# Kernel optimization log

Hardware: AMD Instinct MI355X
Metric: run time of the kernel (lower is better)

Reference implementation:

```python
import jax, jax.numpy as jnp
import numpy as np

N, E, H, D_IN, L, G, T = 50000, 800000, 64, 64, 4, 128, 1

def _w(key, shape, fan_in):
    return jax.random.normal(key, shape, dtype=jnp.float32) / np.sqrt(fan_in)

def setup_inputs() -> dict:
    key = jax.random.key(0)
    ks = jax.random.split(key, 24)
    inp = {
        'x': jax.random.normal(ks[0], (N, D_IN), dtype=jnp.float32),
        'w': jax.random.normal(ks[1], (E, 1), dtype=jnp.float32),
        'src': jax.random.randint(ks[2], (E,), 0, N, dtype=jnp.int32),
        'dst': jax.random.randint(ks[3], (E,), 0, N, dtype=jnp.int32),
        'graph_id': jnp.sort(jax.random.randint(ks[4], (N,), 0, G, dtype=jnp.int32)),
        # input MLP (1 layer, last_activation None; SiLU applied in input_node_func)
        'W_in': _w(ks[5], (D_IN, H), D_IN), 'b_in': jnp.zeros((H,), jnp.float32),
        # per-layer message MLP: (2H+1 -> H -> H), SiLU mid and last
        'msg_W1': _w(ks[6], (L, 2 * H + 1, H), 2 * H + 1), 'msg_b1': jnp.zeros((L, H), jnp.float32),
        'msg_W2': _w(ks[7], (L, H, H), H), 'msg_b2': jnp.zeros((L, H), jnp.float32),
        # per-layer update MLP: (H -> H -> H), SiLU mid, last None
        'upd_W1': _w(ks[8], (L, H, H), H), 'upd_b1': jnp.zeros((L, H), jnp.float32),
        'upd_W2': _w(ks[9], (L, H, H), H), 'upd_b2': jnp.zeros((L, H), jnp.float32),
        # node-wise output MLP: (H -> H -> H), SiLU mid, last None
        'out_W1': _w(ks[10], (H, H), H), 'out_b1': jnp.zeros((H,), jnp.float32),
        'out_W2': _w(ks[11], (H, H), H), 'out_b2': jnp.zeros((H,), jnp.float32),
        # readout MLP: (3H -> H -> T), SiLU mid, last None
        'ro_W1': _w(ks[12], (3 * H, H), 3 * H), 'ro_b1': jnp.zeros((H,), jnp.float32),
        'ro_W2': _w(ks[13], (H, T), H), 'ro_b2': jnp.zeros((T,), jnp.float32),
    }
    return inp

def reference(x, w, src, dst, graph_id, W_in, b_in, msg_W1, msg_b1, msg_W2, msg_b2,
              upd_W1, upd_b1, upd_W2, upd_b2, out_W1, out_b1, out_W2, out_b2,
              ro_W1, ro_b1, ro_W2, ro_b2):
    silu = jax.nn.silu
    f = silu(x @ W_in + b_in)                                   # [N, H]
    sq = w * w                                                  # [E, 1]
    for l in range(L):
        mi = jnp.concatenate([f[src], f[dst], sq], axis=-1)     # [E, 2H+1]
        msg = silu(silu(mi @ msg_W1[l] + msg_b1[l]) @ msg_W2[l] + msg_b2[l])
        m = msg * jax.nn.sigmoid(msg)                           # gated message
        m_sum = jax.ops.segment_sum(m, dst, num_segments=N)     # scatter-sum to dst
        h_new = silu((m_sum + f) @ upd_W1[l] + upd_b1[l]) @ upd_W2[l] + upd_b2[l]
        f = h_new + f                                           # residual
    f = silu(f @ out_W1 + out_b1) @ out_W2 + out_b2             # node-wise output
    g_sum = jax.ops.segment_sum(f, graph_id, num_segments=G)
    cnt = jax.ops.segment_sum(jnp.ones((N, 1), f.dtype), graph_id, num_segments=G)
    g_mean = g_sum / jnp.maximum(cnt, 1.0)
    g_max = jax.ops.segment_max(f, graph_id, num_segments=G)
    readout = jnp.concatenate([g_sum, g_mean, g_max], axis=-1)  # [G, 3H]
    return silu(readout @ ro_W1 + ro_b1) @ ro_W2 + ro_b2        # [G, T]
```

## Files before the change

kernel.cpp:

```cpp
#include <hip/hip_runtime.h>

#define NN 50000
#define EE 800000
#define GG 128
#define LL 4
#define SCAN_B 196

typedef __bf16 bf16x8 __attribute__((ext_vector_type(8)));
typedef float  f32x4  __attribute__((ext_vector_type(4)));

__device__ __forceinline__ float silu_f(float x){
    float t = __builtin_amdgcn_exp2f(-1.44269504f * x);
    return x * __builtin_amdgcn_rcpf(1.0f + t);
}
__device__ __forceinline__ unsigned fenc(float v){
    unsigned u = __float_as_uint(v);
    return (u & 0x80000000u) ? ~u : (u | 0x80000000u);
}
__device__ __forceinline__ float fdec(unsigned u){
    return (u & 0x80000000u) ? __uint_as_float(u & 0x7fffffffu) : __uint_as_float(~u);
}

__global__ __launch_bounds__(256) void pack_k(
        const float* __restrict__ msgW1, const float* __restrict__ msgW2,
        const float* __restrict__ updW1, const float* __restrict__ updW2,
        const float* __restrict__ outW1, const float* __restrict__ outW2,
        const float* __restrict__ W_in, __bf16* __restrict__ pk){
    int m = blockIdx.x;
    const float* src;
    if(m<20){
        int l=m/5, r=m%5;
        if(r==0)      src = msgW1 + (size_t)l*129*64;
        else if(r==1) src = msgW1 + (size_t)l*129*64 + 64*64;
        else if(r==2) src = msgW2 + (size_t)l*64*64;
        else if(r==3) src = updW1 + (size_t)l*64*64;
        else          src = updW2 + (size_t)l*64*64;
    } else if(m==20) src=outW1; else if(m==21) src=outW2; else src=W_in;
    __bf16* dst = pk + (size_t)m*4096;
    int tid=threadIdx.x;
    #pragma unroll
    for(int i=0;i<16;++i){
        int idx = tid*16+i;
        int frag = idx>>9, lane=(idx>>3)&63, j=idx&7;
        int s=frag>>2, ng=frag&3, q=lane>>4, nn=lane&15;
        dst[idx] = (__bf16)src[(32*s+8*q+j)*64 + 16*ng + nn];
    }
}
__device__ __forceinline__ bf16x8 ldfrag(const __bf16* pk, int s, int ng, int lane){
    return *(const bf16x8*)&pk[(((s*4+ng)*64 + lane))*8];
}

__global__ __launch_bounds__(256) void input_mfma(const float* __restrict__ x,
        const __bf16* __restrict__ pkW, const float* __restrict__ bg,
        float* __restrict__ f, __bf16* __restrict__ f16, int N){
    int tid=threadIdx.x, wid=tid>>6, lane=tid&63;
    int q=lane>>4, nn=lane&15;
    bf16x8 Bf[2][4];
    #pragma unroll
    for(int s=0;s<2;++s)
        #pragma unroll
        for(int ng=0;ng<4;++ng) Bf[s][ng]=ldfrag(pkW,s,ng,lane);
    float bias[4];
    #pragma unroll
    for(int ng=0;ng<4;++ng) bias[ng]=bg[16*ng+nn];

    int ntiles=(N+15)/16;
    int gw=gridDim.x*4;
    for(int t=blockIdx.x*4+wid; t<ntiles; t+=gw){
        int m=t*16+nn; int mc=(m<N)?m:(N-1);
        float4 a0=*(const float4*)&x[(size_t)mc*64 + 8*q];
        float4 a1=*(const float4*)&x[(size_t)mc*64 + 8*q + 4];
        float4 a2=*(const float4*)&x[(size_t)mc*64 + 32 + 8*q];
        float4 a3=*(const float4*)&x[(size_t)mc*64 + 32 + 8*q + 4];
        bf16x8 af0, af1;
        af0[0]=(__bf16)a0.x; af0[1]=(__bf16)a0.y; af0[2]=(__bf16)a0.z; af0[3]=(__bf16)a0.w;
        af0[4]=(__bf16)a1.x; af0[5]=(__bf16)a1.y; af0[6]=(__bf16)a1.z; af0[7]=(__bf16)a1.w;
        af1[0]=(__bf16)a2.x; af1[1]=(__bf16)a2.y; af1[2]=(__bf16)a2.z; af1[3]=(__bf16)a2.w;
        af1[4]=(__bf16)a3.x; af1[5]=(__bf16)a3.y; af1[6]=(__bf16)a3.z; af1[7]=(__bf16)a3.w;
        #pragma unroll
        for(int ng=0;ng<4;++ng){
            f32x4 acc; acc[0]=bias[ng]; acc[1]=bias[ng]; acc[2]=bias[ng]; acc[3]=bias[ng];
            acc=__builtin_amdgcn_mfma_f32_16x16x32_bf16(af0,Bf[0][ng],acc,0,0,0);
            acc=__builtin_amdgcn_mfma_f32_16x16x32_bf16(af1,Bf[1][ng],acc,0,0,0);
            #pragma unroll
            for(int r=0;r<4;++r){
                int row=t*16+4*q+r;
                if(row<N){
                    float o=silu_f(acc[r]);
                    f[(size_t)row*64+16*ng+nn]=o;
                    f16[(size_t)row*64+16*ng+nn]=(__bf16)o;
                }
            }
        }
    }
}

__global__ void hist_k(const int* __restrict__ dst, int* __restrict__ deg, int E){
    int e=blockIdx.x*blockDim.x+threadIdx.x;
    if(e<E) atomicAdd(&deg[dst[e]],1);
}

__global__ __launch_bounds__(256) void scan1_k(const int* __restrict__ deg, int* __restrict__ curs,
        int* __restrict__ bsum, int N){
    __shared__ int sv[256];
    int tid=threadIdx.x;
    int idx=blockIdx.x*256+tid;
    int v=(idx<N)?deg[idx]:0;
    sv[tid]=v; __syncthreads();
    #pragma unroll
    for(int off=1; off<256; off<<=1){
        int a=(tid>=off)?sv[tid-off]:0;
        __syncthreads(); sv[tid]+=a; __syncthreads();
    }
    if(idx<N) curs[idx]=sv[tid]-v;
    if(tid==255) bsum[blockIdx.x]=sv[255];
}
__global__ __launch_bounds__(256) void scan2_k(int* __restrict__ bsum, int B){
    __shared__ int sv[256];
    int tid=threadIdx.x;
    int v=(tid<B)?bsum[tid]:0;
    sv[tid]=v; __syncthreads();
    #pragma unroll
    for(int off=1; off<256; off<<=1){
        int a=(tid>=off)?sv[tid-off]:0;
        __syncthreads(); sv[tid]+=a; __syncthreads();
    }
    if(tid<B) bsum[tid]=sv[tid]-v;
}
__global__ __launch_bounds__(256) void scan3_k(int* __restrict__ curs, const int* __restrict__ bsum, int N){
    int idx=blockIdx.x*256+threadIdx.x;
    if(idx<N) curs[idx]+=bsum[blockIdx.x];
}

__global__ void fill_k(const int* __restrict__ src, const int* __restrict__ dst,
                       const float* __restrict__ w, int* __restrict__ cursor,
                       int4* __restrict__ meta, int E){
    int e=blockIdx.x*blockDim.x+threadIdx.x;
    if(e<E){
        int d=dst[e];
        int r=atomicAdd(&cursor[d],1);
        float ww=w[e];
        int4 v; v.x=src[e]; v.y=d; v.z=__float_as_int(ww*ww); v.w=0;
        meta[r]=v;
    }
}

__global__ __launch_bounds__(256) void xy_mfma(const __bf16* __restrict__ f16,
        const __bf16* __restrict__ pkA, const __bf16* __restrict__ pkB,
        const float* __restrict__ b1, __bf16* __restrict__ XY, int N){
    int tid=threadIdx.x, wid=tid>>6, lane=tid&63;
    int q=lane>>4, nn=lane&15;
    bf16x8 Bf[2][8];
    #pragma unroll
    for(int s=0;s<2;++s){
        #pragma unroll
        for(int ng=0;ng<4;++ng){ Bf[s][ng]=ldfrag(pkA,s,ng,lane); Bf[s][4+ng]=ldfrag(pkB,s,ng,lane); }
    }
    float bias[8];
    #pragma unroll
    for(int ng=0;ng<8;++ng) bias[ng]=(ng<4)?0.f:b1[16*(ng-4)+nn];
    int ntiles=(N+15)/16;
    int gw=gridDim.x*4;
    for(int t=blockIdx.x*4+wid; t<ntiles; t+=gw){
        int row=t*16+nn; if(row>=N) row=N-1;
        bf16x8 a0=*(const bf16x8*)&f16[(size_t)row*64 + 8*q];
        bf16x8 a1=*(const bf16x8*)&f16[(size_t)row*64 + 32 + 8*q];
        #pragma unroll
        for(int ng=0;ng<8;++ng){
            f32x4 acc; acc[0]=bias[ng]; acc[1]=bias[ng]; acc[2]=bias[ng]; acc[3]=bias[ng];
            acc=__builtin_amdgcn_mfma_f32_16x16x32_bf16(a0,Bf[0][ng],acc,0,0,0);
            acc=__builtin_amdgcn_mfma_f32_16x16x32_bf16(a1,Bf[1][ng],acc,0,0,0);
            #pragma unroll
            for(int r=0;r<4;++r){
                int orow=t*16+4*q+r;
                if(orow<N) XY[(size_t)orow*128 + 16*ng + nn]=(__bf16)acc[r];
            }
        }
    }
}

__global__ __launch_bounds__(256) void edge_mfma3(
        const __bf16* __restrict__ XY, const int4* __restrict__ meta,
        const __bf16* __restrict__ pkW2,
        const float* __restrict__ W1, const float* __restrict__ b2,
        float* __restrict__ msum, int E){
    int tid=threadIdx.x, wid=tid>>6, lane=tid&63;
    int q=lane>>4, nn=lane&15;

    bf16x8 B2f[2][4];
    #pragma unroll
    for(int s=0;s<2;++s)
        #pragma unroll
        for(int ng=0;ng<4;++ng) B2f[s][ng]=ldfrag(pkW2,s,ng,lane);
    float w128lo[8], w128hi[8];
    #pragma unroll
    for(int j=0;j<8;++j){
        w128lo[j]=W1[128*64 + 8*q+j];
        w128hi[j]=W1[128*64 + 32+8*q+j];
    }
    float bias2[4];
    #pragma unroll
    for(int ng=0;ng<4;++ng) bias2[ng]=b2[16*ng+nn];

    __shared__ __bf16 sm16[4][32][66];

    int ntiles=E/32;
    int nw=gridDim.x*4;
    int chunk=(ntiles+nw-1)/nw;
    int wgl=blockIdx.x*4+wid;
    int t0=wgl*chunk, t1=t0+chunk; if(t1>ntiles) t1=ntiles;
    if(t0>=t1) return;

    int4 mv = meta[(size_t)t0*32 + (lane&31)];
    bf16x8 gx0lo,gx0hi,gy0lo,gy0hi,gx1lo,gx1hi,gy1lo,gy1hi;
    {
        int se0=__shfl(mv.x, nn,64),    de0=__shfl(mv.y, nn,64);
        int se1=__shfl(mv.x, 16+nn,64), de1=__shfl(mv.y, 16+nn,64);
        const __bf16* xp0=XY+(size_t)se0*128; const __bf16* yp0=XY+(size_t)de0*128+64;
        const __bf16* xp1=XY+(size_t)se1*128; const __bf16* yp1=XY+(size_t)de1*128+64;
        gx0lo=*(const bf16x8*)(xp0+8*q); gx0hi=*(const bf16x8*)(xp0+32+8*q);
        gy0lo=*(const bf16x8*)(yp0+8*q); gy0hi=*(const bf16x8*)(yp0+32+8*q);
        gx1lo=*(const bf16x8*)(xp1+8*q); gx1hi=*(const bf16x8*)(xp1+32+8*q);
        gy1lo=*(const bf16x8*)(yp1+8*q); gy1hi=*(const bf16x8*)(yp1+32+8*q);
    }
    int cur=__builtin_amdgcn_readlane(mv.y, 0);
    float vsum=0.f;

    for(int t=t0;t<t1;++t){
        bool hasn = (t+1<t1);
        int4 mvn = mv;
        if(hasn) mvn = meta[(size_t)(t+1)*32 + (lane&31)];

        int d_ = mv.y;
        float w2v = __int_as_float(mv.z);

        {
            float w2 = __shfl(w2v, nn, 64);
            bf16x8 a20, a21;
            #pragma unroll
            for(int j=0;j<8;++j){
                float hlo=(float)gx0lo[j] + (float)gy0lo[j] + w2*w128lo[j];
                float hhi=(float)gx0hi[j] + (float)gy0hi[j] + w2*w128hi[j];
                a20[j]=(__bf16)silu_f(hlo);
                a21[j]=(__bf16)silu_f(hhi);
            }
            f32x4 acc2[4];
            #pragma unroll
            for(int ng=0;ng<4;++ng){ f32x4 c; c[0]=bias2[ng]; c[1]=bias2[ng]; c[2]=bias2[ng]; c[3]=bias2[ng]; acc2[ng]=c; }
            #pragma unroll
            for(int ng=0;ng<4;++ng){
                acc2[ng]=__builtin_amdgcn_mfma_f32_16x16x32_bf16(a20,B2f[0][ng],acc2[ng],0,0,0);
                acc2[ng]=__builtin_amdgcn_mfma_f32_16x16x32_bf16(a21,B2f[1][ng],acc2[ng],0,0,0);
            }
            #pragma unroll
            for(int ng=0;ng<4;++ng)
                #pragma unroll
                for(int r=0;r<4;++r)
                    sm16[wid][4*q+r][16*ng+nn]=(__bf16)silu_f(silu_f(acc2[ng][r]));
        }
        {
            float w2 = __shfl(w2v, 16+nn, 64);
            bf16x8 a20, a21;
            #pragma unroll
            for(int j=0;j<8;++j){
                float hlo=(float)gx1lo[j] + (float)gy1lo[j] + w2*w128lo[j];
                float hhi=(float)gx1hi[j] + (float)gy1hi[j] + w2*w128hi[j];
                a20[j]=(__bf16)silu_f(hlo);
                a21[j]=(__bf16)silu_f(hhi);
            }
            f32x4 acc2[4];
            #pragma unroll
            for(int ng=0;ng<4;++ng){ f32x4 c; c[0]=bias2[ng]; c[1]=bias2[ng]; c[2]=bias2[ng]; c[3]=bias2[ng]; acc2[ng]=c; }
            #pragma unroll
            for(int ng=0;ng<4;++ng){
                acc2[ng]=__builtin_amdgcn_mfma_f32_16x16x32_bf16(a20,B2f[0][ng],acc2[ng],0,0,0);
                acc2[ng]=__builtin_amdgcn_mfma_f32_16x16x32_bf16(a21,B2f[1][ng],acc2[ng],0,0,0);
            }
            #pragma unroll
            for(int ng=0;ng<4;++ng)
                #pragma unroll
                for(int r=0;r<4;++r)
                    sm16[wid][16+4*q+r][16*ng+nn]=(__bf16)silu_f(silu_f(acc2[ng][r]));
        }
        asm volatile("" ::: "memory");

        if(hasn){
            int se0=__shfl(mvn.x, nn,64),    de0=__shfl(mvn.y, nn,64);
            int se1=__shfl(mvn.x, 16+nn,64), de1=__shfl(mvn.y, 16+nn,64);
            const __bf16* xp0=XY+(size_t)se0*128; const __bf16* yp0=XY+(size_t)de0*128+64;
            const __bf16* xp1=XY+(size_t)se1*128; const __bf16* yp1=XY+(size_t)de1*128+64;
            gx0lo=*(const bf16x8*)(xp0+8*q); gx0hi=*(const bf16x8*)(xp0+32+8*q);
            gy0lo=*(const bf16x8*)(yp0+8*q); gy0hi=*(const bf16x8*)(yp0+32+8*q);
            gx1lo=*(const bf16x8*)(xp1+8*q); gx1hi=*(const bf16x8*)(xp1+32+8*q);
            gy1lo=*(const bf16x8*)(yp1+8*q); gy1hi=*(const bf16x8*)(yp1+32+8*q);
        }

        #pragma unroll
        for(int r=0;r<32;++r){
            int dr=__builtin_amdgcn_readlane(d_, r);
            if(dr!=cur){
                atomicAdd(&msum[(size_t)cur*64+lane], vsum);
                vsum=0.f; cur=dr;
            }
            vsum+=(float)sm16[wid][r][lane];
        }
        asm volatile("" ::: "memory");
        mv = mvn;
    }
    atomicAdd(&msum[(size_t)cur*64+lane], vsum);
}

__global__ __launch_bounds__(256) void node_mfma(const float* __restrict__ A, const float* __restrict__ F,
        const __bf16* __restrict__ pkW1, const float* __restrict__ b1,
        const __bf16* __restrict__ pkW2, const float* __restrict__ b2,
        float* __restrict__ out, __bf16* __restrict__ out16, int N){
    int tid=threadIdx.x, wid=tid>>6, lane=tid&63;
    int q=lane>>4, nn=lane&15;

    bf16x8 B1f[2][4], B2f[2][4];
    #pragma unroll
    for(int s=0;s<2;++s)
        #pragma unroll
        for(int ng=0;ng<4;++ng){ B1f[s][ng]=ldfrag(pkW1,s,ng,lane); B2f[s][ng]=ldfrag(pkW2,s,ng,lane); }
    float bias1[4], bias2[4];
    #pragma unroll
    for(int ng=0;ng<4;++ng){ bias1[ng]=b1[16*ng+nn]; bias2[ng]=b2[16*ng+nn]; }

    __shared__ __align__(16) __bf16 sh1[4][16][72];
    __shared__ __align__(16) float sF[4][16][68];
    bool hasF = (F != nullptr);

    int ntiles=(N+15)/16;
    int gw=gridDim.x*4;
    for(int t=blockIdx.x*4+wid; t<ntiles; t+=gw){
        int m=t*16+nn;
        int mc=(m<N)?m:(N-1);
        float4 a0=*(const float4*)&A[(size_t)mc*64 + 8*q];
        float4 a1=*(const float4*)&A[(size_t)mc*64 + 8*q + 4];
        float4 a2=*(const float4*)&A[(size_t)mc*64 + 32 + 8*q];
        float4 a3=*(const float4*)&A[(size_t)mc*64 + 32 + 8*q + 4];
        if(hasF){
            float4 f0=*(const float4*)&F[(size_t)mc*64 + 8*q];
            float4 f1=*(const float4*)&F[(size_t)mc*64 + 8*q + 4];
            float4 f2_=*(const float4*)&F[(size_t)mc*64 + 32 + 8*q];
            float4 f3=*(const float4*)&F[(size_t)mc*64 + 32 + 8*q + 4];
            a0.x+=f0.x; a0.y+=f0.y; a0.z+=f0.z; a0.w+=f0.w;
            a1.x+=f1.x; a1.y+=f1.y; a1.z+=f1.z; a1.w+=f1.w;
            a2.x+=f2_.x; a2.y+=f2_.y; a2.z+=f2_.z; a2.w+=f2_.w;
            a3.x+=f3.x; a3.y+=f3.y; a3.z+=f3.z; a3.w+=f3.w;
            *(float4*)&sF[wid][nn][8*q]   = f0;
            *(float4*)&sF[wid][nn][8*q+4] = f1;
            *(float4*)&sF[wid][nn][32+8*q]   = f2_;
            *(float4*)&sF[wid][nn][32+8*q+4] = f3;
        }
        bf16x8 af0, af1;
        af0[0]=(__bf16)a0.x; af0[1]=(__bf16)a0.y; af0[2]=(__bf16)a0.z; af0[3]=(__bf16)a0.w;
        af0[4]=(__bf16)a1.x; af0[5]=(__bf16)a1.y; af0[6]=(__bf16)a1.z; af0[7]=(__bf16)a1.w;
        af1[0]=(__bf16)a2.x; af1[1]=(__bf16)a2.y; af1[2]=(__bf16)a2.z; af1[3]=(__bf16)a2.w;
        af1[4]=(__bf16)a3.x; af1[5]=(__bf16)a3.y; af1[6]=(__bf16)a3.z; af1[7]=(__bf16)a3.w;

        f32x4 acc[4];
        #pragma unroll
        for(int ng=0;ng<4;++ng){ f32x4 c; c[0]=bias1[ng]; c[1]=bias1[ng]; c[2]=bias1[ng]; c[3]=bias1[ng]; acc[ng]=c; }
        #pragma unroll
        for(int ng=0;ng<4;++ng){
            acc[ng]=__builtin_amdgcn_mfma_f32_16x16x32_bf16(af0,B1f[0][ng],acc[ng],0,0,0);
            acc[ng]=__builtin_amdgcn_mfma_f32_16x16x32_bf16(af1,B1f[1][ng],acc[ng],0,0,0);
        }
        #pragma unroll
        for(int ng=0;ng<4;++ng)
            #pragma unroll
            for(int r=0;r<4;++r)
                sh1[wid][4*q+r][16*ng+nn]=(__bf16)silu_f(acc[ng][r]);
        asm volatile("" ::: "memory");
        bf16x8 a20=*(const bf16x8*)&sh1[wid][nn][8*q];
        bf16x8 a21=*(const bf16x8*)&sh1[wid][nn][32+8*q];
        f32x4 acc2[4];
        #pragma unroll
        for(int ng=0;ng<4;++ng){ f32x4 c; c[0]=bias2[ng]; c[1]=bias2[ng]; c[2]=bias2[ng]; c[3]=bias2[ng]; acc2[ng]=c; }
        #pragma unroll
        for(int ng=0;ng<4;++ng){
            acc2[ng]=__builtin_amdgcn_mfma_f32_16x16x32_bf16(a20,B2f[0][ng],acc2[ng],0,0,0);
            acc2[ng]=__builtin_amdgcn_mfma_f32_16x16x32_bf16(a21,B2f[1][ng],acc2[ng],0,0,0);
        }
        #pragma unroll
        for(int ng=0;ng<4;++ng)
            #pragma unroll
            for(int r=0;r<4;++r){
                int row=t*16+4*q+r;
                if(row<N){
                    float o=acc2[ng][r];
                    if(hasF) o += sF[wid][4*q+r][16*ng+nn];
                    out[(size_t)row*64 + 16*ng + nn]=o;
                    if(out16) out16[(size_t)row*64 + 16*ng + nn]=(__bf16)o;
                }
            }
        asm volatile("" ::: "memory");
    }
}

__global__ __launch_bounds__(256) void seg_reduce_sorted(const float* __restrict__ f2, const int* __restrict__ gid,
        float* __restrict__ gsum, unsigned* __restrict__ gmaxu, float* __restrict__ cnt, int N){
    int wgl=blockIdx.x*4 + (threadIdx.x>>6);
    int lane=threadIdx.x&63;
    int W=gridDim.x*4;
    int chunk=(N+W-1)/W;
    int n0=wgl*chunk;
    int n1=n0+chunk; if(n1>N) n1=N;
    if(n0>=n1) return;
    int cur=gid[n0];
    float s=0.f, mx=-__builtin_inff(), c=0.f;
    for(int n=n0;n<n1;++n){
        int g=gid[n];
        float v=f2[(size_t)n*64+lane];
        if(g!=cur){
            atomicAdd(&gsum[(size_t)cur*64+lane], s);
            atomicMax(&gmaxu[(size_t)cur*64+lane], fenc(mx));
            if(lane==0) atomicAdd(&cnt[cur], c);
            s=0.f; mx=-__builtin_inff(); c=0.f; cur=g;
        }
        s+=v; mx=fmaxf(mx,v); c+=1.f;
    }
    atomicAdd(&gsum[(size_t)cur*64+lane], s);
    atomicMax(&gmaxu[(size_t)cur*64+lane], fenc(mx));
    if(lane==0) atomicAdd(&cnt[cur], c);
}

__global__ __launch_bounds__(256) void readout_k(const float* __restrict__ gsum, const unsigned* __restrict__ gmaxu,
        const float* __restrict__ cnt,
        const float* __restrict__ W1, const float* __restrict__ b1,
        const float* __restrict__ W2, const float* __restrict__ b2,
        float* __restrict__ out, int G){
    __shared__ __align__(16) float sr[4][192];
    int tid=threadIdx.x, wid=tid>>6, lane=tid&63;
    int g=blockIdx.x*4+wid;
    if(g<G){
        float s_=gsum[g*64+lane];
        float c=cnt[g];
        float mean=s_/fmaxf(c,1.0f);
        float mx=fdec(gmaxu[g*64+lane]);
        sr[wid][lane]=s_; sr[wid][64+lane]=mean; sr[wid][128+lane]=mx;
    }
    __syncthreads();
    if(g<G){
        float h=b1[lane];
        for(int k=0;k<192;k+=4){
            float4 r4=*(const float4*)&sr[wid][k];
            h += r4.x*W1[(k+0)*64+lane] + r4.y*W1[(k+1)*64+lane]
               + r4.z*W1[(k+2)*64+lane] + r4.w*W1[(k+3)*64+lane];
        }
        h=silu_f(h);
        float p=h*W2[lane];
        #pragma unroll
        for(int off=32;off>0;off>>=1) p += __shfl_down(p, off, 64);
        if(lane==0) out[g]=p+b2[0];
    }
}

extern "C" void kernel_launch(void* const* d_in, const int* in_sizes, int n_in,
                              void* d_out, int out_size, void* d_ws, size_t ws_size,
                              hipStream_t stream){
    const float* x     = (const float*)d_in[0];
    const float* w     = (const float*)d_in[1];
    const int*   src   = (const int*)d_in[2];
    const int*   dst   = (const int*)d_in[3];
    const int*   gid   = (const int*)d_in[4];
    const float* W_in  = (const float*)d_in[5];
    const float* b_in  = (const float*)d_in[6];
    const float* msgW1 = (const float*)d_in[7];
    const float* msgb1 = (const float*)d_in[8];
    const float* msgW2 = (const float*)d_in[9];
    const float* msgb2 = (const float*)d_in[10];
    const float* updW1 = (const float*)d_in[11];
    const float* updb1 = (const float*)d_in[12];
    const float* updW2 = (const float*)d_in[13];
    const float* updb2 = (const float*)d_in[14];
    const float* outW1 = (const float*)d_in[15];
    const float* outb1 = (const float*)d_in[16];
    const float* outW2 = (const float*)d_in[17];
    const float* outb2 = (const float*)d_in[18];
    const float* roW1  = (const float*)d_in[19];
    const float* rob1  = (const float*)d_in[20];
    const float* roW2  = (const float*)d_in[21];
    const float* rob2  = (const float*)d_in[22];

    float*  f     = (float*)d_ws;
    float*  msum  = f + (size_t)NN*64;
    float*  f2    = msum;
    __bf16* f16   = (__bf16*)(msum + (size_t)NN*64);
    __bf16* XY    = f16 + (size_t)NN*64;
    int4*   meta  = (int4*)(XY + (size_t)NN*128);
    __bf16* pk    = (__bf16*)(meta + EE);
    int*    deg   = (int*)(pk + 23*4096);
    int*    curs  = deg + 50048;
    int*    bsum  = curs + 50048;
    float*  gsum  = (float*)(bsum + 256);
    unsigned* gmaxu = (unsigned*)(gsum + GG*64);
    float*  cnt   = (float*)(gmaxu + GG*64);

    pack_k<<<dim3(23),dim3(256),0,stream>>>(msgW1, msgW2, updW1, updW2, outW1, outW2, W_in, pk);

    hipMemsetAsync(deg, 0, 50048*sizeof(int), stream);
    hist_k<<<dim3((EE+255)/256),dim3(256),0,stream>>>(dst, deg, EE);
    scan1_k<<<dim3(SCAN_B),dim3(256),0,stream>>>(deg, curs, bsum, NN);
    scan2_k<<<dim3(1),dim3(256),0,stream>>>(bsum, SCAN_B);
    scan3_k<<<dim3(SCAN_B),dim3(256),0,stream>>>(curs, bsum, NN);
    fill_k<<<dim3((EE+255)/256),dim3(256),0,stream>>>(src, dst, w, curs, meta, EE);

    input_mfma<<<dim3(782),dim3(256),0,stream>>>(x, pk + (size_t)22*4096, b_in, f, f16, NN);
    for(int l=0;l<LL;++l){
        xy_mfma<<<dim3(512),dim3(256),0,stream>>>(f16,
            pk + (size_t)(5*l+0)*4096, pk + (size_t)(5*l+1)*4096, msgb1 + l*64, XY, NN);
        hipMemsetAsync(msum, 0, (size_t)NN*64*sizeof(float), stream);
        edge_mfma3<<<dim3(1024),dim3(256),0,stream>>>(XY, meta,
            pk + (size_t)(5*l+2)*4096,
            msgW1 + (size_t)l*129*64, msgb2 + l*64, msum, EE);
        node_mfma<<<dim3(782),dim3(256),0,stream>>>(msum, f,
            pk + (size_t)(5*l+3)*4096, updb1 + l*64,
            pk + (size_t)(5*l+4)*4096, updb2 + l*64, f, f16, NN);
    }
    node_mfma<<<dim3(782),dim3(256),0,stream>>>(f, nullptr,
        pk + (size_t)20*4096, outb1, pk + (size_t)21*4096, outb2, f2, nullptr, NN);
    hipMemsetAsync(gsum, 0, (size_t)(GG*64*2 + GG)*sizeof(float), stream);
    seg_reduce_sorted<<<dim3(256),dim3(256),0,stream>>>(f2, gid, gsum, gmaxu, cnt, NN);
    readout_k<<<dim3(32),dim3(256),0,stream>>>(gsum, gmaxu, cnt, roW1, rob1, roW2, rob2, (float*)d_out, GG);
}
```

Measured before the change: 575.2 us.

## Fuse msum zeroing into xy kernel and restructure edge kernel pipeline

Removes the per-layer hipMemsetAsync of the message-sum buffer by zeroing it inside xy_mfma, whose grid is raised to one 16-row tile per wave. The edge kernel now computes both halves' first-layer activations before issuing the next tile's gathers, then runs the MFMAs. It writes results to shared memory as packed 4-wide bf16 stores in a permuted column layout, read back through a lane-to-column remap. The edge grid is doubled, giving shorter per-wave chunks, more parallelism and more boundary atomics.

```diff
diff --git a/kernel.cpp b/kernel.cpp
--- a/kernel.cpp
+++ b/kernel.cpp
@@ -7,6 +7,7 @@
 #define SCAN_B 196
 
 typedef __bf16 bf16x8 __attribute__((ext_vector_type(8)));
+typedef __bf16 bf16x4 __attribute__((ext_vector_type(4)));
 typedef float  f32x4  __attribute__((ext_vector_type(4)));
 
 __device__ __forceinline__ float silu_f(float x){
@@ -147,7 +148,8 @@
 
 __global__ __launch_bounds__(256) void xy_mfma(const __bf16* __restrict__ f16,
         const __bf16* __restrict__ pkA, const __bf16* __restrict__ pkB,
-        const float* __restrict__ b1, __bf16* __restrict__ XY, int N){
+        const float* __restrict__ b1, __bf16* __restrict__ XY,
+        float* __restrict__ msum, int N){
     int tid=threadIdx.x, wid=tid>>6, lane=tid&63;
     int q=lane>>4, nn=lane&15;
     bf16x8 Bf[2][8];
@@ -165,6 +167,17 @@
         int row=t*16+nn; if(row>=N) row=N-1;
         bf16x8 a0=*(const bf16x8*)&f16[(size_t)row*64 + 8*q];
         bf16x8 a1=*(const bf16x8*)&f16[(size_t)row*64 + 32 + 8*q];
+        {
+            float4 z; z.x=0.f; z.y=0.f; z.z=0.f; z.w=0.f;
+            float4* mz=(float4*)(msum + (size_t)t*1024);
+            int lim=(t*16+16<=N)?4:0;
+            if(lim){
+                #pragma unroll
+                for(int i=0;i<4;++i) mz[i*64+lane]=z;
+            } else {
+                for(int rr=t*16; rr<N; ++rr) msum[(size_t)rr*64+lane]=0.f;
+            }
+        }
         #pragma unroll
         for(int ng=0;ng<8;++ng){
             f32x4 acc; acc[0]=bias[ng]; acc[1]=bias[ng]; acc[2]=bias[ng]; acc[3]=bias[ng];
@@ -179,7 +192,7 @@
     }
 }
 
-__global__ __launch_bounds__(256) void edge_mfma3(
+__global__ __launch_bounds__(256) void edge_mfma4(
         const __bf16* __restrict__ XY, const int4* __restrict__ meta,
         const __bf16* __restrict__ pkW2,
         const float* __restrict__ W1, const float* __restrict__ b2,
@@ -202,7 +215,8 @@
     #pragma unroll
     for(int ng=0;ng<4;++ng) bias2[ng]=b2[16*ng+nn];
 
-    __shared__ __bf16 sm16[4][32][66];
+    __shared__ __align__(16) __bf16 sm16[4][32][68];
+    int cpos = 4*(lane&15) + (lane>>4);
 
     int ntiles=E/32;
     int nw=gridDim.x*4;
@@ -234,56 +248,18 @@
         int d_ = mv.y;
         float w2v = __int_as_float(mv.z);
 
+        bf16x8 A0lo,A0hi,A1lo,A1hi;
         {
-            float w2 = __shfl(w2v, nn, 64);
-            bf16x8 a20, a21;
+            float w2a = __shfl(w2v, nn, 64);
+            float w2b = __shfl(w2v, 16+nn, 64);
             #pragma unroll
             for(int j=0;j<8;++j){
-                float hlo=(float)gx0lo[j] + (float)gy0lo[j] + w2*w128lo[j];
-                float hhi=(float)gx0hi[j] + (float)gy0hi[j] + w2*w128hi[j];
-                a20[j]=(__bf16)silu_f(hlo);
-                a21[j]=(__bf16)silu_f(hhi);
-            }
-            f32x4 acc2[4];
-            #pragma unroll
-            for(int ng=0;ng<4;++ng){ f32x4 c; c[0]=bias2[ng]; c[1]=bias2[ng]; c[2]=bias2[ng]; c[3]=bias2[ng]; acc2[ng]=c; }
-            #pragma unroll
-            for(int ng=0;ng<4;++ng){
-                acc2[ng]=__builtin_amdgcn_mfma_f32_16x16x32_bf16(a20,B2f[0][ng],acc2[ng],0,0,0);
-                acc2[ng]=__builtin_amdgcn_mfma_f32_16x16x32_bf16(a21,B2f[1][ng],acc2[ng],0,0,0);
-            }
-            #pragma unroll
-            for(int ng=0;ng<4;++ng)
-                #pragma unroll
-                for(int r=0;r<4;++r)
-                    sm16[wid][4*q+r][16*ng+nn]=(__bf16)silu_f(silu_f(acc2[ng][r]));
-        }
-        {
-            float w2 = __shfl(w2v, 16+nn, 64);
-            bf16x8 a20, a21;
-            #pragma unroll
-            for(int j=0;j<8;++j){
-                float hlo=(float)gx1lo[j] + (float)gy1lo[j] + w2*w128lo[j];
-                float hhi=(float)gx1hi[j] + (float)gy1hi[j] + w2*w128hi[j];
-                a20[j]=(__bf16)silu_f(hlo);
-                a21[j]=(__bf16)silu_f(hhi);
-            }
-            f32x4 acc2[4];
-            #pragma unroll
-            for(int ng=0;ng<4;++ng){ f32x4 c; c[0]=bias2[ng]; c[1]=bias2[ng]; c[2]=bias2[ng]; c[3]=bias2[ng]; acc2[ng]=c; }
-            #pragma unroll
-            for(int ng=0;ng<4;++ng){
-                acc2[ng]=__builtin_amdgcn_mfma_f32_16x16x32_bf16(a20,B2f[0][ng],acc2[ng],0,0,0);
-                acc2[ng]=__builtin_amdgcn_mfma_f32_16x16x32_bf16(a21,B2f[1][ng],acc2[ng],0,0,0);
-            }
-            #pragma unroll
-            for(int ng=0;ng<4;++ng)
-                #pragma unroll
-                for(int r=0;r<4;++r)
-                    sm16[wid][16+4*q+r][16*ng+nn]=(__bf16)silu_f(silu_f(acc2[ng][r]));
-        }
-        asm volatile("" ::: "memory");
-
+                A0lo[j]=(__bf16)silu_f((float)gx0lo[j] + (float)gy0lo[j] + w2a*w128lo[j]);
+                A0hi[j]=(__bf16)silu_f((float)gx0hi[j] + (float)gy0hi[j] + w2a*w128hi[j]);
+                A1lo[j]=(__bf16)silu_f((float)gx1lo[j] + (float)gy1lo[j] + w2b*w128lo[j]);
+                A1hi[j]=(__bf16)silu_f((float)gx1hi[j] + (float)gy1hi[j] + w2b*w128hi[j]);
+            }
+        }
         if(hasn){
             int se0=__shfl(mvn.x, nn,64),    de0=__shfl(mvn.y, nn,64);
             int se1=__shfl(mvn.x, 16+nn,64), de1=__shfl(mvn.y, 16+nn,64);
@@ -294,7 +270,27 @@
             gx1lo=*(const bf16x8*)(xp1+8*q); gx1hi=*(const bf16x8*)(xp1+32+8*q);
             gy1lo=*(const bf16x8*)(yp1+8*q); gy1hi=*(const bf16x8*)(yp1+32+8*q);
         }
-
+        #pragma unroll
+        for(int h=0;h<2;++h){
+            bf16x8 alo = h ? A1lo : A0lo;
+            bf16x8 ahi = h ? A1hi : A0hi;
+            f32x4 acc2[4];
+            #pragma unroll
+            for(int ng=0;ng<4;++ng){ f32x4 c; c[0]=bias2[ng]; c[1]=bias2[ng]; c[2]=bias2[ng]; c[3]=bias2[ng]; acc2[ng]=c; }
+            #pragma unroll
+            for(int ng=0;ng<4;++ng){
+                acc2[ng]=__builtin_amdgcn_mfma_f32_16x16x32_bf16(alo,B2f[0][ng],acc2[ng],0,0,0);
+                acc2[ng]=__builtin_amdgcn_mfma_f32_16x16x32_bf16(ahi,B2f[1][ng],acc2[ng],0,0,0);
+            }
+            #pragma unroll
+            for(int r=0;r<4;++r){
+                bf16x4 pv;
+                #pragma unroll
+                for(int ng=0;ng<4;++ng) pv[ng]=(__bf16)silu_f(silu_f(acc2[ng][r]));
+                *(bf16x4*)&sm16[wid][16*h+4*q+r][4*nn] = pv;
+            }
+        }
+        asm volatile("" ::: "memory");
         #pragma unroll
         for(int r=0;r<32;++r){
             int dr=__builtin_amdgcn_readlane(d_, r);
@@ -302,7 +298,7 @@
                 atomicAdd(&msum[(size_t)cur*64+lane], vsum);
                 vsum=0.f; cur=dr;
             }
-            vsum+=(float)sm16[wid][r][lane];
+            vsum+=(float)sm16[wid][r][cpos];
         }
         asm volatile("" ::: "memory");
         mv = mvn;
@@ -509,10 +505,9 @@
 
     input_mfma<<<dim3(782),dim3(256),0,stream>>>(x, pk + (size_t)22*4096, b_in, f, f16, NN);
     for(int l=0;l<LL;++l){
-        xy_mfma<<<dim3(512),dim3(256),0,stream>>>(f16,
-            pk + (size_t)(5*l+0)*4096, pk + (size_t)(5*l+1)*4096, msgb1 + l*64, XY, NN);
-        hipMemsetAsync(msum, 0, (size_t)NN*64*sizeof(float), stream);
-        edge_mfma3<<<dim3(1024),dim3(256),0,stream>>>(XY, meta,
+        xy_mfma<<<dim3(782),dim3(256),0,stream>>>(f16,
+            pk + (size_t)(5*l+0)*4096, pk + (size_t)(5*l+1)*4096, msgb1 + l*64, XY, msum, NN);
+        edge_mfma4<<<dim3(2048),dim3(256),0,stream>>>(XY, meta,
             pk + (size_t)(5*l+2)*4096,
             msgW1 + (size_t)l*129*64, msgb2 + l*64, msum, EE);
         node_mfma<<<dim3(782),dim3(256),0,stream>>>(msum, f,
```

New measurement: 593.8 us. 3.2% more time.
